# Optimization experiments

Hardware: AMD Instinct MI355X
Metric: run time of the kernel (lower is better)

Reference implementation:

```python
import jax, jax.numpy as jnp
import numpy as np

D_MODEL = 1024
NUM_HEADS = 16
HEAD_DIM = D_MODEL // NUM_HEADS


def setup_inputs() -> dict:
    key = jax.random.key(0)
    k_x, k_wqkv, k_bqkv, k_wo, k_bo = jax.random.split(key, 5)
    B, T = 4, 2048
    s = 1.0 / np.sqrt(D_MODEL)
    return {
        "x": jax.random.normal(k_x, (B, T, D_MODEL), dtype=jnp.float32),
        "w_qkv": jax.random.uniform(k_wqkv, (D_MODEL, 3 * D_MODEL), jnp.float32, -s, s),
        "b_qkv": jax.random.uniform(k_bqkv, (3 * D_MODEL,), jnp.float32, -s, s),
        "w_out": jax.random.uniform(k_wo, (D_MODEL, D_MODEL), jnp.float32, -s, s),
        "b_out": jax.random.uniform(k_bo, (D_MODEL,), jnp.float32, -s, s),
    }


def reference(x, w_qkv, b_qkv, w_out, b_out):
    B, T, _ = x.shape
    H, Dh = NUM_HEADS, HEAD_DIM
    scale = Dh ** -0.5
    qkv = x @ w_qkv + b_qkv                       # [B,T,3D]
    qkv = qkv.reshape(B, T, 3, H, Dh)
    q = jnp.transpose(qkv[:, :, 0], (0, 2, 1, 3))  # [B,H,T,Dh]
    k = jnp.transpose(qkv[:, :, 1], (0, 2, 1, 3))
    v = jnp.transpose(qkv[:, :, 2], (0, 2, 1, 3))
    scores = jnp.einsum('bhqd,bhkd->bhqk', q, k) * scale
    causal = jnp.tril(jnp.ones((T, T), dtype=bool))
    scores = jnp.where(causal, scores, -jnp.inf)
    w = jax.nn.softmax(scores, axis=-1)
    out = jnp.einsum('bhqk,bhkd->bhqd', w, v)     # [B,H,T,Dh]
    out = jnp.transpose(out, (0, 2, 1, 3)).reshape(B, T, H * Dh)
    return out @ w_out + b_out
```

## Files before the change

### kernel.cpp

```cpp
#include <hip/hip_runtime.h>

typedef unsigned short u16;
typedef unsigned u32;
typedef float f32x4 __attribute__((ext_vector_type(4)));
typedef __bf16 bf16x8 __attribute__((ext_vector_type(8)));
typedef __bf16 bf16x2 __attribute__((ext_vector_type(2)));
typedef u32 u32x4 __attribute__((ext_vector_type(4)));
typedef u16 u16x4 __attribute__((ext_vector_type(4)));
typedef int i32x2 __attribute__((ext_vector_type(2)));

#define MFMA_16x16x32(a, b, c) __builtin_amdgcn_mfma_f32_16x16x32_bf16((a), (b), (c), 0, 0, 0)

#if __has_builtin(__builtin_amdgcn_exp2f)
#define EXP2(x) __builtin_amdgcn_exp2f(x)
#else
#define EXP2(x) exp2f(x)
#endif


__device__ __forceinline__ u16 f2bf(float f) {
  unsigned u = __builtin_bit_cast(unsigned, f);
  unsigned r = ((u >> 16) & 1u) + 0x7FFFu;
  return (u16)((u + r) >> 16);
}

__device__ __forceinline__ u32 pk2(float x, float y) {
  bf16x2 v = {(__bf16)x, (__bf16)y};
  return __builtin_bit_cast(u32, v);
}

__device__ __forceinline__ void gload16(const void* g, void* l) {
  __builtin_amdgcn_global_load_lds(
      (const __attribute__((address_space(1))) void*)g,
      (__attribute__((address_space(3))) void*)l, 16, 0, 0);
}



__global__ void cvt_to_bf16(const float* __restrict__ in, u16* __restrict__ out, int n) {
  const int s = blockIdx.x * 256 + threadIdx.x;
  if (s * 8 >= n) return;
  const int l = s & 63, f = (s >> 6) & 7, kb = (s >> 9) & 31, R = s >> 14;
  const int rr = ((f >> 2) << 6) + ((f & 3) << 4) + (l & 15);
  const int row = (R << 7) + rr;
  const int k = (kb << 5) + ((l >> 4) << 3);
  const float* src = in + (size_t)row * 1024 + k;
  const f32x4 a = *(const f32x4*)src;
  const f32x4 b = *(const f32x4*)(src + 4);
  u16x4 u0, u1;
#pragma unroll
  for (int j = 0; j < 4; ++j) { u0[j] = f2bf(a[j]); u1[j] = f2bf(b[j]); }
  *(u16x4*)(out + (size_t)s * 8) = u0;
  *(u16x4*)(out + (size_t)s * 8 + 4) = u1;
}

__global__ void transpose_cvt(const float* __restrict__ in, u16* __restrict__ out,
                              int rows, int cols) {
  __shared__ float t[64][65];
  const int rb = blockIdx.y * 64, cb = blockIdx.x * 64;
  for (int i = threadIdx.x; i < 4096; i += 256) {
    const int r = i >> 6, c = i & 63;
    t[r][c] = in[(size_t)(rb + r) * cols + cb + c];
  }
  __syncthreads();
  for (int u = threadIdx.x; u < 512; u += 256) {
    const int c = u >> 3, k8 = u & 7;
    const int nrow = cb + c;
    const int kg = rb + k8 * 8;
    const int R = nrow >> 7, rr = nrow & 127;
    const int fB = ((rr >> 6) << 2) + ((rr >> 4) & 3);
    const int kb = kg >> 5, koct = (kg >> 3) & 3;
    u16* dst = out + (((size_t)R * 32 + kb) * 8 + fB) * 512 + ((koct << 4) + (rr & 15)) * 8;
    u16x4 u0, u1;
#pragma unroll
    for (int j = 0; j < 4; ++j) {
      u0[j] = f2bf(t[k8 * 8 + j][c]);
      u1[j] = f2bf(t[k8 * 8 + 4 + j][c]);
    }
    *(u16x4*)dst = u0;
    *(u16x4*)(dst + 4) = u1;
  }
}

template <int EPI>
__global__ __launch_bounds__(256, 4) void gemm_bt(
    const u16* __restrict__ A, const u16* __restrict__ Bt, int K,
    const float* __restrict__ bias,
    u16* __restrict__ oq, u16* __restrict__ ok, u16* __restrict__ ov,
    float* __restrict__ of, int N, int nbx) {
  __shared__ __align__(16) u16 As[2][4096];
  __shared__ __align__(16) u16 Bs[2][4096];
  const int tid = threadIdx.x;
  const int lane = tid & 63, w = tid >> 6;
  const int g = lane >> 4, cc = lane & 15;
  const int wr = w >> 1, wc = w & 1;

  const int cpx = gridDim.x >> 3;
  const int bid = ((int)blockIdx.x & 7) * cpx + ((int)blockIdx.x >> 3);
  const int bx = bid % nbx, by = bid / nbx;

  const u16* pa = A + ((size_t)by * 256 + w) * 512 + lane * 8;
  const u16* pb = Bt + ((size_t)bx * 256 + w) * 512 + lane * 8;

  f32x4 acc[4][4] = {};

#define STG(S, T)                                              \
  do {                                                         \
    const size_t o_ = (size_t)(T) * 4096;                      \
    gload16(pa + o_, &As[S][w * 512 + lane * 8]);              \
    gload16(pa + o_ + 2048, &As[S][(w + 4) * 512 + lane * 8]); \
    gload16(pb + o_, &Bs[S][w * 512 + lane * 8]);              \
    gload16(pb + o_ + 2048, &Bs[S][(w + 4) * 512 + lane * 8]); \
  } while (0)

#define CMP(S, DOSTG, T)                                                 \
  do {                                                                   \
    bf16x8 af[4], bf[4];                                                 \
    _Pragma("unroll") for (int mi = 0; mi < 4; ++mi)                     \
        af[mi] = *(const bf16x8*)&As[S][(wr * 4 + mi) * 512 + lane * 8]; \
    _Pragma("unroll") for (int ni = 0; ni < 4; ++ni)                     \
        bf[ni] = *(const bf16x8*)&Bs[S][(wc * 4 + ni) * 512 + lane * 8]; \
    if (DOSTG) STG(S ^ 1, T);                                            \
    __builtin_amdgcn_s_setprio(1);                                       \
    _Pragma("unroll") for (int mi = 0; mi < 4; ++mi)                     \
      _Pragma("unroll") for (int ni = 0; ni < 4; ++ni)                   \
          acc[mi][ni] = MFMA_16x16x32(af[mi], bf[ni], acc[mi][ni]);      \
    __builtin_amdgcn_s_setprio(0);                                       \
  } while (0)

  STG(0, 0);
  __syncthreads();

  const int np = (K >> 5) >> 1;
  for (int p = 0; p < np - 1; ++p) {
    CMP(0, true, 2 * p + 1);
    __syncthreads();
    CMP(1, true, 2 * p + 2);
    __syncthreads();
  }
  CMP(0, true, 2 * np - 1);
  __syncthreads();
  CMP(1, false, 0);

#undef STG
#undef CMP

  const int m00 = by * 128 + wr * 64 + 4 * g;
  const int n00 = bx * 128 + wc * 64;
#pragma unroll
  for (int ni = 0; ni < 4; ++ni) {
    const int n = n00 + ni * 16 + cc;
    const float bn = bias[n];
    if constexpr (EPI == 0) {
      const int which = n >> 10;
      const int d = n & 1023;
      const int h = d >> 6, dh = d & 63;
      const int dcf = dh >> 5, gf = (dh >> 3) & 3, e = dh & 7;
      const int niv = dh >> 4, ccv = dh & 15;
#pragma unroll
      for (int mi = 0; mi < 4; ++mi) {
        const int mb = m00 + mi * 16;
        const int b = mb >> 11, t0b = mb & 2047;
        const int bh2 = b * 16 + h;
        const int kt = t0b >> 7, tr = t0b & 127;
        if (which == 2) {
          const int kk0 = (tr & ~12) | ((tr & 4) << 1) | ((tr & 8) >> 1);
          const int ko = kk0 >> 5, gv = (kk0 >> 3) & 3, ev = kk0 & 7;
          u16x4 pk;
#pragma unroll
          for (int r = 0; r < 4; ++r) pk[r] = f2bf(acc[mi][ni][r] + bn);
          *(u16x4*)&ov[(((size_t)bh2 * 16 + kt) * 16 + ko * 4 + niv) * 512 +
                       ((gv << 4) + ccv) * 8 + ev] = pk;
        } else if (which == 1) {
          const int ki = tr >> 4;
          u16* dst = ok + (((size_t)bh2 * 16 + kt) * 16 + dcf * 8 + ki) * 512 +
                     ((gf << 4) + (tr & 15)) * 8 + e;
#pragma unroll
          for (int r = 0; r < 4; ++r) dst[r * 8] = f2bf(acc[mi][ni][r] + bn);
        } else {
          const int wf = tr >> 5, mif = (tr >> 4) & 1;
          u16* dst = oq + (((size_t)bh2 * 16 + kt) * 16 + wf * 4 + mif * 2 + dcf) * 512 +
                     ((gf << 4) + (tr & 15)) * 8 + e;
#pragma unroll
          for (int r = 0; r < 4; ++r) dst[r * 8] = f2bf(acc[mi][ni][r] + bn);
        }
      }
    } else {
#pragma unroll
      for (int mi = 0; mi < 4; ++mi) {
        const int m = m00 + mi * 16;
#pragma unroll
        for (int r = 0; r < 4; ++r) of[(size_t)(m + r) * N + n] = acc[mi][ni][r] + bn;
      }
    }
  }
}

__global__ __launch_bounds__(256, 2) void flash_attn(
    const u16* __restrict__ Qb, const u16* __restrict__ Kb,
    const u16* __restrict__ Vt, u16* __restrict__ Ob) {
  __shared__ __align__(16) u16 Ks[2][8192];
  __shared__ __align__(16) u16 Vs[2][8192];

  const int bid = blockIdx.x;
  const int tq4 = bid >> 6, t0 = tq4 & 3, ti = tq4 >> 2;
  const int qt = (ti == 0) ? 15 - t0 : (ti == 1) ? 8 + t0 : (ti == 2) ? 7 - t0 : t0;
  const int bh = bid & 63;
  const int tid = threadIdx.x;
  const int lane = tid & 63, w = tid >> 6;
  const int g = lane >> 4, cc = lane & 15;
  const int q0 = qt * 128 + w * 32;
  const int qq0 = w * 32 + cc, qq1 = w * 32 + 16 + cc;

  bf16x8 bq[2][2];
  {
    const u16* qp = Qb + (((size_t)bh * 16 + qt) * 16 + w * 4) * 512 + lane * 8;
#pragma unroll
    for (int mi = 0; mi < 2; ++mi)
#pragma unroll
      for (int dc = 0; dc < 2; ++dc)
        bq[mi][dc] = *(const bf16x8*)(qp + (mi * 2 + dc) * 512);
  }

  const char* kp = (const char*)Kb + (size_t)bh * 262144 + w * 1024 + lane * 16;
  const char* vp = (const char*)Vt + (size_t)bh * 262144 + w * 1024 + lane * 16;

  const u32x4 ones_u = {0x3F803F80u, 0x3F803F80u, 0x3F803F80u, 0x3F803F80u};
  const bf16x8 ones = __builtin_bit_cast(bf16x8, ones_u);

  f32x4 ac0[4] = {}, ac1[4] = {};
  f32x4 ls0 = {}, ls1 = {};
  float m0 = -1e30f, m1 = -1e30f;
  const float sc = 0.18033688011112042f;

  u32x4 kreg[4], vreg[4];
#pragma unroll
  for (int i = 0; i < 4; ++i) {
    kreg[i] = *(const u32x4*)(kp + i * 4096);
    vreg[i] = *(const u32x4*)(vp + i * 4096);
  }
  kp += 16384;
  vp += 16384;
#pragma unroll
  for (int i = 0; i < 4; ++i) {
    *(u32x4*)&Ks[0][(i * 4 + w) * 512 + lane * 8] = kreg[i];
    *(u32x4*)&Vs[0][(i * 4 + w) * 512 + lane * 8] = vreg[i];
  }
  __syncthreads();

#define SMPV(S, MR, LS, AC, B)                                              \
  do {                                                                      \
    float t4[8];                                                            \
    _Pragma("unroll") for (int ki = 0; ki < 8; ++ki)                        \
        t4[ki] = fmaxf(fmaxf(S[ki][0], S[ki][1]), fmaxf(S[ki][2], S[ki][3])); \
    float mx = fmaxf(fmaxf(fmaxf(t4[0], t4[1]), fmaxf(t4[2], t4[3])),       \
                     fmaxf(fmaxf(t4[4], t4[5]), fmaxf(t4[6], t4[7])));      \
    mx = fmaxf(mx, __shfl_xor(mx, 16));                                     \
    mx = fmaxf(mx, __shfl_xor(mx, 32));                                     \
    const float pm = mx * sc;                                               \
    if (!__all(pm - MR <= 8.f)) {                                           \
      const float mn = fmaxf(MR, pm);                                       \
      const float sf = EXP2(MR - mn);                                       \
      MR = mn;                                                              \
      float sfr[4];                                                        \
      _Pragma("unroll") for (int r = 0; r < 4; ++r)                         \
          sfr[r] = __shfl(sf, (lane & 48) + 4 * g + r);                     \
      _Pragma("unroll") for (int r = 0; r < 4; ++r) LS[r] *= sfr[r];        \
      _Pragma("unroll") for (int ni = 0; ni < 4; ++ni)                      \
        _Pragma("unroll") for (int r = 0; r < 4; ++r) AC[ni][r] *= sfr[r];  \
    }                                                                       \
    const float mcur = MR;                                                  \
    _Pragma("unroll") for (int ko = 0; ko < 4; ++ko) {                      \
      f32x4 pe, po;                                                         \
      _Pragma("unroll") for (int r = 0; r < 4; ++r) {                       \
        pe[r] = EXP2(__builtin_fmaf(S[2 * ko][r], sc, -mcur));              \
        po[r] = EXP2(__builtin_fmaf(S[2 * ko + 1][r], sc, -mcur));          \
      }                                                                     \
      const u32 aw = pk2(pe[0], pe[1]), bw2 = pk2(pe[2], pe[3]);            \
      const u32 cw = pk2(po[0], po[1]), dw = pk2(po[2], po[3]);             \
      const i32x2 s1_ = __builtin_amdgcn_permlane32_swap((int)aw, (int)cw, false, false); \
      const i32x2 s2_ = __builtin_amdgcn_permlane32_swap((int)bw2, (int)dw, false, false); \
      const u32x4 wv = {(u32)s1_[0], (u32)s2_[0], (u32)s1_[1], (u32)s2_[1]}; \
      const bf16x8 pf = __builtin_bit_cast(bf16x8, wv);                     \
      __builtin_amdgcn_s_setprio(1);                                        \
      _Pragma("unroll") for (int ni = 0; ni < 4; ++ni) {                    \
        const bf16x8 bv = *(const bf16x8*)&Vs[B][(ko * 4 + ni) * 512 + lane * 8]; \
        AC[ni] = MFMA_16x16x32(pf, bv, AC[ni]);                             \
      }                                                                     \
      LS = MFMA_16x16x32(pf, ones, LS);                                     \
      __builtin_amdgcn_s_setprio(0);                                        \
    }                                                                       \
  } while (0)

#define COMPUTE(B, KT)                                                      \
  do {                                                                      \
    f32x4 s0[8] = {}, s1[8] = {};                                           \
    __builtin_amdgcn_s_setprio(1);                                          \
    _Pragma("unroll") for (int dc = 0; dc < 2; ++dc) {                      \
      _Pragma("unroll") for (int ki = 0; ki < 8; ++ki) {                    \
        const bf16x8 ak =                                                   \
            *(const bf16x8*)&Ks[B][(dc * 8 + ki) * 512 + lane * 8];         \
        s0[ki] = MFMA_16x16x32(ak, bq[0][dc], s0[ki]);                      \
        s1[ki] = MFMA_16x16x32(ak, bq[1][dc], s1[ki]);                      \
      }                                                                     \
    }                                                                       \
    __builtin_amdgcn_s_setprio(0);                                          \
    if ((KT) == qt) {                                                       \
      _Pragma("unroll") for (int ki = 0; ki < 8; ++ki) {                    \
        const int kb_ = ki * 16 + 4 * g;                                    \
        _Pragma("unroll") for (int r = 0; r < 4; ++r) {                     \
          if (kb_ + r > qq0) s0[ki][r] = -1e30f;                            \
          if (kb_ + r > qq1) s1[ki][r] = -1e30f;                            \
        }                                                                   \
      }                                                                     \
    }                                                                       \
    SMPV(s0, m0, ls0, ac0, B);                                              \
    SMPV(s1, m1, ls1, ac1, B);                                              \
  } while (0)

#define ITER(KT, B)                                                         \
  do {                                                                      \
    const bool pf_ = (KT) < qt;                                             \
    if (pf_) {                                                              \
      _Pragma("unroll") for (int i = 0; i < 4; ++i) {                       \
        kreg[i] = *(const u32x4*)(kp + i * 4096);                           \
        vreg[i] = *(const u32x4*)(vp + i * 4096);                           \
      }                                                                     \
      kp += 16384;                                                          \
      vp += 16384;                                                          \
    }                                                                       \
    COMPUTE(B, KT);                                                         \
    if (pf_) {                                                              \
      _Pragma("unroll") for (int i = 0; i < 4; ++i) {                       \
        *(u32x4*)&Ks[(B) ^ 1][(i * 4 + w) * 512 + lane * 8] = kreg[i];      \
        *(u32x4*)&Vs[(B) ^ 1][(i * 4 + w) * 512 + lane * 8] = vreg[i];      \
      }                                                                     \
    }                                                                       \
    __syncthreads();                                                        \
  } while (0)

  int kt = 0;
  while (kt + 1 <= qt) {
    ITER(kt, 0);
    ITER(kt + 1, 1);
    kt += 2;
  }
  if (kt <= qt) ITER(kt, 0);

#undef ITER
#undef COMPUTE
#undef SMPV

  const int b = bh >> 4, h = bh & 15;
  auto epi = [&](const f32x4(&AC)[4], const f32x4& LS, int mi) {
    f32x4 inv;
#pragma unroll
    for (int r = 0; r < 4; ++r) inv[r] = 1.f / LS[r];
#pragma unroll
    for (int ni = 0; ni < 4; ++ni) {
      const int d = h * 64 + ni * 16 + cc;
      const int kbA = d >> 5, koA = (d >> 3) & 3, eA = d & 7;
#pragma unroll
      for (int r = 0; r < 4; ++r) {
        const int tq = q0 + mi * 16 + 4 * g + r;
        const int row = b * 2048 + tq;
        const int R = row >> 7, rr = row & 127;
        const int fA = ((rr >> 6) << 2) + ((rr >> 4) & 3);
        Ob[(((size_t)R * 32 + kbA) * 8 + fA) * 512 + ((koA << 4) + (rr & 15)) * 8 + eA] =
            f2bf(AC[ni][r] * inv[r]);
      }
    }
  };
  epi(ac0, ls0, 0);
  epi(ac1, ls1, 1);
}


extern "C" void kernel_launch(void* const* d_in, const int* in_sizes, int n_in,
                              void* d_out, int out_size, void* d_ws, size_t ws_size,
                              hipStream_t stream) {
  const float* x     = (const float*)d_in[0];
  const float* w_qkv = (const float*)d_in[1];
  const float* b_qkv = (const float*)d_in[2];
  const float* w_out = (const float*)d_in[3];
  const float* b_out = (const float*)d_in[4];
  float* out = (float*)d_out;
  char* ws = (char*)d_ws;

  u16* xb    = (u16*)(ws + 0);
  u16* wqkvT = (u16*)(ws + 16777216);
  u16* woutT = (u16*)(ws + 23068672);
  u16* qbuf  = (u16*)(ws + 25165824);
  u16* kbuf  = (u16*)(ws + 41943040);
  u16* vbuf  = (u16*)(ws + 58720256);

  cvt_to_bf16<<<4096, 256, 0, stream>>>(x, xb, 8388608);
  transpose_cvt<<<dim3(48, 16), 256, 0, stream>>>(w_qkv, wqkvT, 1024, 3072);
  transpose_cvt<<<dim3(16, 16), 256, 0, stream>>>(w_out, woutT, 1024, 1024);
  gemm_bt<0><<<24 * 64, 256, 0, stream>>>(xb, wqkvT, 1024, b_qkv,
                                          qbuf, kbuf, vbuf, nullptr, 3072, 24);
  flash_attn<<<1024, 256, 0, stream>>>(qbuf, kbuf, vbuf, xb);
  gemm_bt<1><<<8 * 64, 256, 0, stream>>>(xb, woutT, 1024, b_out,
                                         nullptr, nullptr, nullptr, out, 1024, 8);
}
```

Baseline: 161.8 us.

## Single-buffer K, direct-to-LDS V loads, split QK per m-tile, raise occupancy

The flash attention kernel now keeps K in a single LDS buffer refilled from registers after a barrier. V stays double-buffered but is fetched with direct global-to-LDS loads (gload16), so it no longer passes through registers. The QK^T score computation is split per 16-row m-tile so only one score array is live at a time, and launch bounds go to 3 blocks per SM to raise occupancy. In exchange, each iteration needs two barriers and hand-written waitcnt instructions, which brings in more synchronisation and a risk of ordering bugs.

```diff
diff --git a/kernel.cpp b/kernel.cpp
--- a/kernel.cpp
+++ b/kernel.cpp
@@ -196,10 +196,10 @@
   }
 }
 
-__global__ __launch_bounds__(256, 2) void flash_attn(
+__global__ __launch_bounds__(256, 3) void flash_attn(
     const u16* __restrict__ Qb, const u16* __restrict__ Kb,
     const u16* __restrict__ Vt, u16* __restrict__ Ob) {
-  __shared__ __align__(16) u16 Ks[2][8192];
+  __shared__ __align__(16) u16 Ks[8192];
   __shared__ __align__(16) u16 Vs[2][8192];
 
   const int bid = blockIdx.x;
@@ -210,7 +210,6 @@
   const int lane = tid & 63, w = tid >> 6;
   const int g = lane >> 4, cc = lane & 15;
   const int q0 = qt * 128 + w * 32;
-  const int qq0 = w * 32 + cc, qq1 = w * 32 + 16 + cc;
 
   bf16x8 bq[2][2];
   {
@@ -228,115 +227,120 @@
   const u32x4 ones_u = {0x3F803F80u, 0x3F803F80u, 0x3F803F80u, 0x3F803F80u};
   const bf16x8 ones = __builtin_bit_cast(bf16x8, ones_u);
 
-  f32x4 ac0[4] = {}, ac1[4] = {};
-  f32x4 ls0 = {}, ls1 = {};
-  float m0 = -1e30f, m1 = -1e30f;
+  f32x4 acc[2][4] = {};
+  f32x4 lsum[2] = {};
+  float m_run[2] = {-1e30f, -1e30f};
   const float sc = 0.18033688011112042f;
 
-  u32x4 kreg[4], vreg[4];
-#pragma unroll
-  for (int i = 0; i < 4; ++i) {
-    kreg[i] = *(const u32x4*)(kp + i * 4096);
-    vreg[i] = *(const u32x4*)(vp + i * 4096);
-  }
+  u32x4 kreg[4];
+#pragma unroll
+  for (int i = 0; i < 4; ++i) kreg[i] = *(const u32x4*)(kp + i * 4096);
   kp += 16384;
+#pragma unroll
+  for (int i = 0; i < 4; ++i)
+    gload16(vp + i * 4096, &Vs[0][(i * 4 + w) * 512 + lane * 8]);
   vp += 16384;
 #pragma unroll
-  for (int i = 0; i < 4; ++i) {
-    *(u32x4*)&Ks[0][(i * 4 + w) * 512 + lane * 8] = kreg[i];
-    *(u32x4*)&Vs[0][(i * 4 + w) * 512 + lane * 8] = vreg[i];
+  for (int i = 0; i < 4; ++i)
+    *(u32x4*)&Ks[(i * 4 + w) * 512 + lane * 8] = kreg[i];
+  if (qt > 0) {
+#pragma unroll
+    for (int i = 0; i < 4; ++i) kreg[i] = *(const u32x4*)(kp + i * 4096);
+    kp += 16384;
   }
   __syncthreads();
 
-#define SMPV(S, MR, LS, AC, B)                                              \
-  do {                                                                      \
-    float t4[8];                                                            \
-    _Pragma("unroll") for (int ki = 0; ki < 8; ++ki)                        \
+#define SMPV(S, MR, LS, AC, B)                                                \
+  do {                                                                        \
+    float t4[8];                                                              \
+    _Pragma("unroll") for (int ki = 0; ki < 8; ++ki)                          \
         t4[ki] = fmaxf(fmaxf(S[ki][0], S[ki][1]), fmaxf(S[ki][2], S[ki][3])); \
-    float mx = fmaxf(fmaxf(fmaxf(t4[0], t4[1]), fmaxf(t4[2], t4[3])),       \
-                     fmaxf(fmaxf(t4[4], t4[5]), fmaxf(t4[6], t4[7])));      \
-    mx = fmaxf(mx, __shfl_xor(mx, 16));                                     \
-    mx = fmaxf(mx, __shfl_xor(mx, 32));                                     \
-    const float pm = mx * sc;                                               \
-    if (!__all(pm - MR <= 8.f)) {                                           \
-      const float mn = fmaxf(MR, pm);                                       \
-      const float sf = EXP2(MR - mn);                                       \
-      MR = mn;                                                              \
-      float sfr[4];                                                        \
-      _Pragma("unroll") for (int r = 0; r < 4; ++r)                         \
-          sfr[r] = __shfl(sf, (lane & 48) + 4 * g + r);                     \
-      _Pragma("unroll") for (int r = 0; r < 4; ++r) LS[r] *= sfr[r];        \
-      _Pragma("unroll") for (int ni = 0; ni < 4; ++ni)                      \
-        _Pragma("unroll") for (int r = 0; r < 4; ++r) AC[ni][r] *= sfr[r];  \
-    }                                                                       \
-    const float mcur = MR;                                                  \
-    _Pragma("unroll") for (int ko = 0; ko < 4; ++ko) {                      \
-      f32x4 pe, po;                                                         \
-      _Pragma("unroll") for (int r = 0; r < 4; ++r) {                       \
-        pe[r] = EXP2(__builtin_fmaf(S[2 * ko][r], sc, -mcur));              \
-        po[r] = EXP2(__builtin_fmaf(S[2 * ko + 1][r], sc, -mcur));          \
-      }                                                                     \
-      const u32 aw = pk2(pe[0], pe[1]), bw2 = pk2(pe[2], pe[3]);            \
-      const u32 cw = pk2(po[0], po[1]), dw = pk2(po[2], po[3]);             \
-      const i32x2 s1_ = __builtin_amdgcn_permlane32_swap((int)aw, (int)cw, false, false); \
-      const i32x2 s2_ = __builtin_amdgcn_permlane32_swap((int)bw2, (int)dw, false, false); \
-      const u32x4 wv = {(u32)s1_[0], (u32)s2_[0], (u32)s1_[1], (u32)s2_[1]}; \
-      const bf16x8 pf = __builtin_bit_cast(bf16x8, wv);                     \
-      __builtin_amdgcn_s_setprio(1);                                        \
-      _Pragma("unroll") for (int ni = 0; ni < 4; ++ni) {                    \
-        const bf16x8 bv = *(const bf16x8*)&Vs[B][(ko * 4 + ni) * 512 + lane * 8]; \
-        AC[ni] = MFMA_16x16x32(pf, bv, AC[ni]);                             \
-      }                                                                     \
-      LS = MFMA_16x16x32(pf, ones, LS);                                     \
-      __builtin_amdgcn_s_setprio(0);                                        \
-    }                                                                       \
+    float mx = fmaxf(fmaxf(fmaxf(t4[0], t4[1]), fmaxf(t4[2], t4[3])),         \
+                     fmaxf(fmaxf(t4[4], t4[5]), fmaxf(t4[6], t4[7])));        \
+    mx = fmaxf(mx, __shfl_xor(mx, 16));                                       \
+    mx = fmaxf(mx, __shfl_xor(mx, 32));                                       \
+    const float pm = mx * sc;                                                 \
+    if (!__all(pm - MR <= 8.f)) {                                             \
+      const float mn = fmaxf(MR, pm);                                         \
+      const float sf = EXP2(MR - mn);                                         \
+      MR = mn;                                                                \
+      float sfr[4];                                                           \
+      _Pragma("unroll") for (int r = 0; r < 4; ++r)                           \
+          sfr[r] = __shfl(sf, (lane & 48) + 4 * g + r);                       \
+      _Pragma("unroll") for (int r = 0; r < 4; ++r) LS[r] *= sfr[r];          \
+      _Pragma("unroll") for (int ni = 0; ni < 4; ++ni)                        \
+        _Pragma("unroll") for (int r = 0; r < 4; ++r) AC[ni][r] *= sfr[r];    \
+    }                                                                         \
+    const float mcur = MR;                                                    \
+    _Pragma("unroll") for (int ko = 0; ko < 4; ++ko) {                        \
+      f32x4 pe, po;                                                           \
+      _Pragma("unroll") for (int r = 0; r < 4; ++r) {                         \
+        pe[r] = EXP2(__builtin_fmaf(S[2 * ko][r], sc, -mcur));                \
+        po[r] = EXP2(__builtin_fmaf(S[2 * ko + 1][r], sc, -mcur));            \
+      }                                                                       \
+      const u32 aw = pk2(pe[0], pe[1]), bw2 = pk2(pe[2], pe[3]);              \
+      const u32 cw = pk2(po[0], po[1]), dw = pk2(po[2], po[3]);               \
+      const i32x2 s1_ =                                                       \
+          __builtin_amdgcn_permlane32_swap((int)aw, (int)cw, false, false);   \
+      const i32x2 s2_ =                                                       \
+          __builtin_amdgcn_permlane32_swap((int)bw2, (int)dw, false, false);  \
+      const u32x4 wv = {(u32)s1_[0], (u32)s2_[0], (u32)s1_[1], (u32)s2_[1]};  \
+      const bf16x8 pf = __builtin_bit_cast(bf16x8, wv);                       \
+      __builtin_amdgcn_s_setprio(1);                                          \
+      _Pragma("unroll") for (int ni = 0; ni < 4; ++ni) {                      \
+        const bf16x8 bv =                                                     \
+            *(const bf16x8*)&Vs[B][(ko * 4 + ni) * 512 + lane * 8];           \
+        AC[ni] = MFMA_16x16x32(pf, bv, AC[ni]);                               \
+      }                                                                       \
+      LS = MFMA_16x16x32(pf, ones, LS);                                       \
+      __builtin_amdgcn_s_setprio(0);                                          \
+    }                                                                         \
   } while (0)
 
-#define COMPUTE(B, KT)                                                      \
-  do {                                                                      \
-    f32x4 s0[8] = {}, s1[8] = {};                                           \
-    __builtin_amdgcn_s_setprio(1);                                          \
-    _Pragma("unroll") for (int dc = 0; dc < 2; ++dc) {                      \
-      _Pragma("unroll") for (int ki = 0; ki < 8; ++ki) {                    \
-        const bf16x8 ak =                                                   \
-            *(const bf16x8*)&Ks[B][(dc * 8 + ki) * 512 + lane * 8];         \
-        s0[ki] = MFMA_16x16x32(ak, bq[0][dc], s0[ki]);                      \
-        s1[ki] = MFMA_16x16x32(ak, bq[1][dc], s1[ki]);                      \
-      }                                                                     \
-    }                                                                       \
-    __builtin_amdgcn_s_setprio(0);                                          \
-    if ((KT) == qt) {                                                       \
-      _Pragma("unroll") for (int ki = 0; ki < 8; ++ki) {                    \
-        const int kb_ = ki * 16 + 4 * g;                                    \
-        _Pragma("unroll") for (int r = 0; r < 4; ++r) {                     \
-          if (kb_ + r > qq0) s0[ki][r] = -1e30f;                            \
-          if (kb_ + r > qq1) s1[ki][r] = -1e30f;                            \
-        }                                                                   \
-      }                                                                     \
-    }                                                                       \
-    SMPV(s0, m0, ls0, ac0, B);                                              \
-    SMPV(s1, m1, ls1, ac1, B);                                              \
-  } while (0)
-
-#define ITER(KT, B)                                                         \
-  do {                                                                      \
-    const bool pf_ = (KT) < qt;                                             \
-    if (pf_) {                                                              \
-      _Pragma("unroll") for (int i = 0; i < 4; ++i) {                       \
-        kreg[i] = *(const u32x4*)(kp + i * 4096);                           \
-        vreg[i] = *(const u32x4*)(vp + i * 4096);                           \
-      }                                                                     \
-      kp += 16384;                                                          \
-      vp += 16384;                                                          \
-    }                                                                       \
-    COMPUTE(B, KT);                                                         \
-    if (pf_) {                                                              \
-      _Pragma("unroll") for (int i = 0; i < 4; ++i) {                       \
-        *(u32x4*)&Ks[(B) ^ 1][(i * 4 + w) * 512 + lane * 8] = kreg[i];      \
-        *(u32x4*)&Vs[(B) ^ 1][(i * 4 + w) * 512 + lane * 8] = vreg[i];      \
-      }                                                                     \
-    }                                                                       \
-    __syncthreads();                                                        \
+#define ITER(KT, B)                                                           \
+  do {                                                                        \
+    if ((KT) < qt) {                     \
+      _Pragma("unroll") for (int i = 0; i < 4; ++i)                           \
+          gload16(vp + i * 4096, &Vs[(B) ^ 1][(i * 4 + w) * 512 + lane * 8]); \
+      vp += 16384;                                                            \
+    }                                                                         \
+    _Pragma("unroll") for (int mi = 0; mi < 2; ++mi) {                        \
+      f32x4 s[8] = {};                                                        \
+      __builtin_amdgcn_s_setprio(1);                                          \
+      _Pragma("unroll") for (int dc = 0; dc < 2; ++dc) {                      \
+        const bf16x8 qf = bq[mi][dc];                                         \
+        _Pragma("unroll") for (int ki = 0; ki < 8; ++ki) {                    \
+          const bf16x8 ak =                                                   \
+              *(const bf16x8*)&Ks[(dc * 8 + ki) * 512 + lane * 8];            \
+          s[ki] = MFMA_16x16x32(ak, qf, s[ki]);                               \
+        }                                                                     \
+      }                                                                       \
+      __builtin_amdgcn_s_setprio(0);                                          \
+      if ((KT) == qt) {                                                       \
+        const int qq = w * 32 + mi * 16 + cc;                                 \
+        _Pragma("unroll") for (int ki = 0; ki < 8; ++ki) {                    \
+          const int kb_ = ki * 16 + 4 * g;                                    \
+          _Pragma("unroll") for (int r = 0; r < 4; ++r)                       \
+            if (kb_ + r > qq) s[ki][r] = -1e30f;                              \
+        }                                                                     \
+      }                                                                       \
+      if (mi == 0) SMPV(s, m_run[0], lsum[0], acc[0], B);                     \
+      else SMPV(s, m_run[1], lsum[1], acc[1], B);                             \
+    }                                                                         \
+    if ((KT) < qt) {                                                          \
+      __builtin_amdgcn_s_barrier();            \
+      _Pragma("unroll") for (int i = 0; i < 4; ++i)                           \
+          *(u32x4*)&Ks[(i * 4 + w) * 512 + lane * 8] = kreg[i];               \
+      if ((KT) + 1 < qt) {                                                    \
+        _Pragma("unroll") for (int i = 0; i < 4; ++i)                         \
+            kreg[i] = *(const u32x4*)(kp + i * 4096);                         \
+        kp += 16384;                                                          \
+        asm volatile("s_waitcnt vmcnt(4) lgkmcnt(0)" ::: "memory");           \
+      } else {                                                                \
+        asm volatile("s_waitcnt vmcnt(0) lgkmcnt(0)" ::: "memory");           \
+      }                                                                       \
+      __builtin_amdgcn_s_barrier();                                           \
+    }                                                                         \
   } while (0)
 
   int kt = 0;
@@ -348,14 +352,14 @@
   if (kt <= qt) ITER(kt, 0);
 
 #undef ITER
-#undef COMPUTE
 #undef SMPV
 
   const int b = bh >> 4, h = bh & 15;
-  auto epi = [&](const f32x4(&AC)[4], const f32x4& LS, int mi) {
+#pragma unroll
+  for (int mi = 0; mi < 2; ++mi) {
     f32x4 inv;
 #pragma unroll
-    for (int r = 0; r < 4; ++r) inv[r] = 1.f / LS[r];
+    for (int r = 0; r < 4; ++r) inv[r] = 1.f / lsum[mi][r];
 #pragma unroll
     for (int ni = 0; ni < 4; ++ni) {
       const int d = h * 64 + ni * 16 + cc;
@@ -367,12 +371,10 @@
         const int R = row >> 7, rr = row & 127;
         const int fA = ((rr >> 6) << 2) + ((rr >> 4) & 3);
         Ob[(((size_t)R * 32 + kbA) * 8 + fA) * 512 + ((koA << 4) + (rr & 15)) * 8 + eA] =
-            f2bf(AC[ni][r] * inv[r]);
+            f2bf(acc[mi][ni][r] * inv[r]);
       }
     }
-  };
-  epi(ac0, ls0, 0);
-  epi(ac1, ls1, 1);
+  }
 }
 
 
```

After: 201.7 us. +24.7%, slower.
